# Optimization experiments

Hardware: AMD Instinct MI355X
Metric: run time of the kernel (lower is better)

## Reference

```python
import jax, jax.numpy as jnp
import numpy as np

N_NODES = 50000
NNZ = 1250000
N_EDGES = 1600000
VOCAB = 40000
HIDDEN = 128
LABELS = 2000
NUM_GCN = 2


def setup_inputs() -> dict:
    key = jax.random.key(0)
    ks = jax.random.split(key, 16)
    feat_ids = jax.random.randint(ks[0], (NNZ,), 0, VOCAB, dtype=jnp.int32)
    mid = jnp.sort(jax.random.randint(ks[1], (N_NODES - 1,), 0, NNZ, dtype=jnp.int32))
    offsets = jnp.concatenate([jnp.zeros((1,), jnp.int32), mid, jnp.full((1,), NNZ, jnp.int32)])
    feat_weights = jax.random.uniform(ks[2], (NNZ,), jnp.float32)
    edge_src = jax.random.randint(ks[3], (N_EDGES,), 0, N_NODES, dtype=jnp.int32)
    edge_dst = jax.random.randint(ks[4], (N_EDGES,), 0, N_NODES, dtype=jnp.int32)
    ppi_w = jax.random.uniform(ks[5], (N_EDGES,), jnp.float32)
    self_w = jax.random.uniform(ks[6], (N_EDGES,), jnp.float32)
    # learned params (xavier-ish scaling)
    emb_weight = jax.random.normal(ks[7], (VOCAB, HIDDEN), jnp.float32) * 0.02
    input_bias = jnp.zeros((HIDDEN,), jnp.float32)
    W1 = jax.random.normal(ks[8], (HIDDEN, HIDDEN), jnp.float32) * (1.0 / np.sqrt(HIDDEN))
    b1 = jnp.zeros((HIDDEN,), jnp.float32)
    W2 = jax.random.normal(ks[9], (HIDDEN, HIDDEN), jnp.float32) * (1.0 / np.sqrt(HIDDEN))
    b2 = jnp.zeros((HIDDEN,), jnp.float32)
    Wo = jax.random.normal(ks[10], (HIDDEN, LABELS), jnp.float32) * (1.0 / np.sqrt(HIDDEN))
    bo = jnp.zeros((LABELS,), jnp.float32)
    return {
        'feat_ids': feat_ids, 'offsets': offsets, 'feat_weights': feat_weights,
        'edge_src': edge_src, 'edge_dst': edge_dst, 'ppi_w': ppi_w, 'self_w': self_w,
        'emb_weight': emb_weight, 'input_bias': input_bias,
        'W1': W1, 'b1': b1, 'W2': W2, 'b2': b2, 'Wo': Wo, 'bo': bo,
    }


def _embedding_bag_sum(emb_weight, feat_ids, offsets, feat_weights):
    # EmbeddingBag(mode='sum', include_last_offset=True) with per_sample_weights:
    # bag b sums feat_weights[i] * emb_weight[feat_ids[i]] for i in [offsets[b], offsets[b+1]).
    bag_id = jnp.searchsorted(offsets, jnp.arange(NNZ, dtype=offsets.dtype), side='right') - 1
    vals = emb_weight[feat_ids] * feat_weights[:, None]  # [NNZ, H]
    return jax.ops.segment_sum(vals, bag_id, num_segments=N_NODES)  # [N, H]


def reference(feat_ids, offsets, feat_weights, edge_src, edge_dst, ppi_w, self_w,
              emb_weight, input_bias, W1, b1, W2, b2, Wo, bo):
    # input layer: EmbeddingBag sum + bias -> relu (dropout = identity in eval)
    h = jax.nn.relu(_embedding_bag_sum(emb_weight, feat_ids, offsets, feat_weights) + input_bias)
    for (W, b) in ((W1, b1), (W2, b2)):
        hs = h[edge_src]                                            # gather [E, H]
        res = jax.ops.segment_sum(hs * self_w[:, None], edge_dst, num_segments=N_NODES)
        agg = jax.ops.segment_sum(hs * ppi_w[:, None], edge_dst, num_segments=N_NODES)
        # NodeUpdate: dropout(relu(Linear(ppi_out))) + res  (dropout identity)
        h = jax.nn.relu(agg @ W + b) + res
    return h @ Wo + bo  # [N, LABELS]
```

## Files before the change

### kernel.cpp

```cpp
#include <hip/hip_runtime.h>

#define HID 128

typedef __bf16 bf16x8 __attribute__((ext_vector_type(8)));
typedef float f32x4 __attribute__((ext_vector_type(4)));

__device__ __forceinline__ unsigned short f2bf(float x) {
  unsigned int u = __builtin_bit_cast(unsigned int, x);
  u += 0x7FFFu + ((u >> 16) & 1u);
  return (unsigned short)(u >> 16);
}

__global__ void zero_int_kernel(int* __restrict__ p, int n) {
  int i = blockIdx.x * blockDim.x + threadIdx.x;
  if (i < n) p[i] = 0;
}

__global__ void degree_kernel(const int* __restrict__ dst, int* __restrict__ deg, int n) {
  int i = blockIdx.x * blockDim.x + threadIdx.x;
  if (i < n) atomicAdd(&deg[dst[i]], 1);
}

__global__ void __launch_bounds__(1024) scan_kernel(const int* __restrict__ deg,
                                                    int* __restrict__ eoff, int n) {
  __shared__ int ssum[1024];
  int t = threadIdx.x;
  int chunk = (n + 1023) / 1024;
  int beg = t * chunk;
  int end = min(beg + chunk, n);
  int s = 0;
  for (int i = beg; i < end; ++i) s += deg[i];
  ssum[t] = s;
  __syncthreads();
  for (int off = 1; off < 1024; off <<= 1) {
    int v = (t >= off) ? ssum[t - off] : 0;
    __syncthreads();
    ssum[t] += v;
    __syncthreads();
  }
  int base = (t == 0) ? 0 : ssum[t - 1];
  for (int i = beg; i < end; ++i) { eoff[i] = base; base += deg[i]; }
  if (t == 1023) eoff[n] = base;
}

__global__ void copy_int_kernel(const int* __restrict__ src, int* __restrict__ dst, int n) {
  int i = blockIdx.x * blockDim.x + threadIdx.x;
  if (i < n) dst[i] = src[i];
}

__global__ void scatter_kernel(const int* __restrict__ edst, const int* __restrict__ esrc,
                               const float* __restrict__ ppi, const float* __restrict__ selfw,
                               int* __restrict__ cursor,
                               int* __restrict__ esrc_s, float2* __restrict__ w2, int n) {
  int i = blockIdx.x * blockDim.x + threadIdx.x;
  if (i < n) {
    int d = edst[i];
    int pos = atomicAdd(&cursor[d], 1);
    esrc_s[pos] = esrc[i];
    w2[pos] = make_float2(ppi[i], selfw[i]);
  }
}

__global__ void __launch_bounds__(128) embed_kernel(const int* __restrict__ ids,
                                                    const int* __restrict__ offs,
                                                    const float* __restrict__ fw,
                                                    const float* __restrict__ emb,
                                                    const float* __restrict__ bias,
                                                    float* __restrict__ h) {
  int node = blockIdx.x;
  int t = threadIdx.x;
  int beg = offs[node], end = offs[node + 1];
  float acc = 0.f;
  int i = beg;
  for (; i + 8 <= end; i += 8) {
    int id[8];
    float w[8];
    float v[8];
#pragma unroll
    for (int u = 0; u < 8; ++u) id[u] = ids[i + u];
#pragma unroll
    for (int u = 0; u < 8; ++u) w[u] = fw[i + u];
#pragma unroll
    for (int u = 0; u < 8; ++u) v[u] = emb[(long)id[u] * HID + t];
#pragma unroll
    for (int u = 0; u < 8; ++u) acc += w[u] * v[u];
  }
  for (; i < end; ++i) {
    acc += fw[i] * emb[(long)ids[i] * HID + t];
  }
  acc += bias[t];
  h[(long)node * HID + t] = acc > 0.f ? acc : 0.f;
}

__global__ void __launch_bounds__(128) aggregate_kernel(const float* __restrict__ h,
                                                        const int* __restrict__ eoff,
                                                        const int* __restrict__ esrc_s,
                                                        const float2* __restrict__ w2,
                                                        float* __restrict__ agg,
                                                        float* __restrict__ res) {
  int node = blockIdx.x;
  int t = threadIdx.x;
  int beg = eoff[node], end = eoff[node + 1];
  float a = 0.f, r = 0.f;
  int j = beg;
  for (; j + 8 <= end; j += 8) {
    int s[8];
    float2 w[8];
    float v[8];
#pragma unroll
    for (int u = 0; u < 8; ++u) s[u] = esrc_s[j + u];
#pragma unroll
    for (int u = 0; u < 8; ++u) w[u] = w2[j + u];
#pragma unroll
    for (int u = 0; u < 8; ++u) v[u] = h[(long)s[u] * HID + t];
#pragma unroll
    for (int u = 0; u < 8; ++u) { a += w[u].x * v[u]; r += w[u].y * v[u]; }
  }
  for (; j < end; ++j) {
    int s = esrc_s[j];
    float2 w = w2[j];
    float v = h[(long)s * HID + t];
    a += w.x * v;
    r += w.y * v;
  }
  agg[(long)node * HID + t] = a;
  res[(long)node * HID + t] = r;
}

__global__ void __launch_bounds__(256) update_kernel(const float* __restrict__ agg,
                                                     const float* __restrict__ res,
                                                     const float* __restrict__ W,
                                                     const float* __restrict__ b,
                                                     float* __restrict__ hout, int n_nodes) {
  __shared__ __align__(16) float sW[HID * HID];
  __shared__ float sx[2][HID];
  int t = threadIdx.x & (HID - 1);
  int sub = threadIdx.x >> 7;
  for (int i = threadIdx.x; i < HID * HID / 4; i += 256)
    ((float4*)sW)[i] = ((const float4*)W)[i];
  float bias = b[t];
  __syncthreads();
  for (int node0 = blockIdx.x * 2; node0 < n_nodes; node0 += gridDim.x * 2) {
    int node = node0 + sub;
    bool valid = node < n_nodes;
    if (valid) sx[sub][t] = agg[(long)node * HID + t];
    __syncthreads();
    if (valid) {
      float acc = 0.f;
#pragma unroll 16
      for (int k = 0; k < HID; ++k) acc += sx[sub][k] * sW[k * HID + t];
      float v = acc + bias;
      v = v > 0.f ? v : 0.f;
      hout[(long)node * HID + t] = v + res[(long)node * HID + t];
    }
    __syncthreads();
  }
}

__global__ void transpose_wo_kernel(const float* __restrict__ Wo,
                                    unsigned short* __restrict__ WoT, int labels) {
  int idx = blockIdx.x * 256 + threadIdx.x;
  if (idx < labels * HID) {
    int n = idx >> 7, k = idx & (HID - 1);
    WoT[idx] = f2bf(Wo[(long)k * labels + n]);
  }
}

#define LDK 136

__global__ void __launch_bounds__(256) out_gemm_kernel(const float* __restrict__ h,
                                                       const unsigned short* __restrict__ WoT,
                                                       const float* __restrict__ bo,
                                                       float* __restrict__ out,
                                                       int n_nodes, int labels) {
  __shared__ __align__(16) unsigned short sA[64 * LDK];
  __shared__ __align__(16) unsigned short sB[80 * LDK];
  int m0 = blockIdx.x * 64;
  int n0 = blockIdx.y * 80;
  int tid = threadIdx.x;

  for (int i = tid; i < 64 * 32; i += 256) {
    int r = i >> 5, c4 = i & 31;
    int row = m0 + r;
    if (row >= n_nodes) row = n_nodes - 1;
    float4 v = ((const float4*)(h + (long)row * HID))[c4];
    ushort4 bb;
    bb.x = f2bf(v.x); bb.y = f2bf(v.y); bb.z = f2bf(v.z); bb.w = f2bf(v.w);
    *(ushort4*)&sA[r * LDK + c4 * 4] = bb;
  }
  for (int i = tid; i < 80 * 32; i += 256) {
    int r = i >> 5, c4 = i & 31;
    ushort4 v = ((const ushort4*)(WoT + (long)(n0 + r) * HID))[c4];
    *(ushort4*)&sB[r * LDK + c4 * 4] = v;
  }
  __syncthreads();

  int wave = tid >> 6, lane = tid & 63;
  int lrow = lane & 15, quad = lane >> 4;
  f32x4 acc[5];
#pragma unroll
  for (int c = 0; c < 5; ++c) acc[c] = (f32x4){0.f, 0.f, 0.f, 0.f};

#pragma unroll
  for (int kk = 0; kk < 4; ++kk) {
    bf16x8 af = *(const bf16x8*)&sA[(wave * 16 + lrow) * LDK + kk * 32 + quad * 8];
#pragma unroll
    for (int c = 0; c < 5; ++c) {
      bf16x8 bf = *(const bf16x8*)&sB[(c * 16 + lrow) * LDK + kk * 32 + quad * 8];
      acc[c] = __builtin_amdgcn_mfma_f32_16x16x32_bf16(af, bf, acc[c], 0, 0, 0);
    }
  }

#pragma unroll
  for (int c = 0; c < 5; ++c) {
    int n = n0 + c * 16 + lrow;
    float bias = bo[n];
#pragma unroll
    for (int r = 0; r < 4; ++r) {
      int m = m0 + wave * 16 + quad * 4 + r;
      if (m < n_nodes) out[(long)m * labels + n] = acc[c][r] + bias;
    }
  }
}

extern "C" void kernel_launch(void* const* d_in, const int* in_sizes, int n_in,
                              void* d_out, int out_size, void* d_ws, size_t ws_size,
                              hipStream_t stream) {
  const int* feat_ids = (const int*)d_in[0];
  const int* offsets = (const int*)d_in[1];
  const float* feat_w = (const float*)d_in[2];
  const int* esrc = (const int*)d_in[3];
  const int* edst = (const int*)d_in[4];
  const float* ppi = (const float*)d_in[5];
  const float* selfw = (const float*)d_in[6];
  const float* emb = (const float*)d_in[7];
  const float* ibias = (const float*)d_in[8];
  const float* W1 = (const float*)d_in[9];
  const float* b1 = (const float*)d_in[10];
  const float* W2 = (const float*)d_in[11];
  const float* b2 = (const float*)d_in[12];
  const float* Wo = (const float*)d_in[13];
  const float* bo = (const float*)d_in[14];
  float* out = (float*)d_out;

  int N = in_sizes[1] - 1;
  int E = in_sizes[3];
  int LABELS = in_sizes[14];

  char* ws = (char*)d_ws;
  size_t HN = (size_t)N * HID;
  float* h0 = (float*)ws;                    ws += HN * 4;
  float* agg = (float*)ws;                   ws += HN * 4;
  float* res = (float*)ws;                   ws += HN * 4;
  unsigned short* WoT = (unsigned short*)ws; ws += (size_t)LABELS * HID * 2;
  float2* w2 = (float2*)ws;                  ws += (size_t)E * 8;
  int* deg = (int*)ws;                       ws += (size_t)N * 4;
  int* eoff = (int*)ws;                      ws += (size_t)(N + 1) * 4;
  int* cursor = (int*)ws;                    ws += (size_t)N * 4;
  int* esrc_s = (int*)ws;                    ws += (size_t)E * 4;

  zero_int_kernel<<<(N + 255) / 256, 256, 0, stream>>>(deg, N);
  degree_kernel<<<(E + 255) / 256, 256, 0, stream>>>(edst, deg, E);
  scan_kernel<<<1, 1024, 0, stream>>>(deg, eoff, N);
  copy_int_kernel<<<(N + 255) / 256, 256, 0, stream>>>(eoff, cursor, N);
  scatter_kernel<<<(E + 255) / 256, 256, 0, stream>>>(edst, esrc, ppi, selfw,
                                                      cursor, esrc_s, w2, E);

  embed_kernel<<<N, HID, 0, stream>>>(feat_ids, offsets, feat_w, emb, ibias, h0);
  transpose_wo_kernel<<<(LABELS * HID + 255) / 256, 256, 0, stream>>>(Wo, WoT, LABELS);

  aggregate_kernel<<<N, HID, 0, stream>>>(h0, eoff, esrc_s, w2, agg, res);
  update_kernel<<<1024, 256, 0, stream>>>(agg, res, W1, b1, h0, N);
  aggregate_kernel<<<N, HID, 0, stream>>>(h0, eoff, esrc_s, w2, agg, res);
  update_kernel<<<1024, 256, 0, stream>>>(agg, res, W2, b2, h0, N);

  dim3 g((N + 63) / 64, LABELS / 80);
  out_gemm_kernel<<<g, 256, 0, stream>>>(h0, WoT, bo, out, N, LABELS);
}
```

Baseline: 1.421 ms.

## Store node features and embedding table in bf16; pack edge records into int4

Converts the embedding table and the node hidden states to bf16, so the embedding-bag and aggregation gathers move half the bytes. Each wavefront now handles one node with two features per lane. Edge source, ppi weight and self weight are packed into a single 16-byte record so one load fetches all three. The output GEMM reads the bf16 hidden state directly instead of converting from fp32. The cost is an extra cast pass over the embedding table and reduced precision in the intermediate activations, including the residual term.

New measurement: 1.281 ms. 9.8% less time.

```diff
diff --git a/kernel.cpp b/kernel.cpp
--- a/kernel.cpp
+++ b/kernel.cpp
@@ -9,6 +9,9 @@
   unsigned int u = __builtin_bit_cast(unsigned int, x);
   u += 0x7FFFu + ((u >> 16) & 1u);
   return (unsigned short)(u >> 16);
+}
+__device__ __forceinline__ float bf2f(unsigned short x) {
+  return __builtin_bit_cast(float, (unsigned int)x << 16);
 }
 
 __global__ void zero_int_kernel(int* __restrict__ p, int n) {
@@ -50,88 +53,111 @@
 
 __global__ void scatter_kernel(const int* __restrict__ edst, const int* __restrict__ esrc,
                                const float* __restrict__ ppi, const float* __restrict__ selfw,
-                               int* __restrict__ cursor,
-                               int* __restrict__ esrc_s, float2* __restrict__ w2, int n) {
+                               int* __restrict__ cursor, int4* __restrict__ edges, int n) {
   int i = blockIdx.x * blockDim.x + threadIdx.x;
   if (i < n) {
     int d = edst[i];
     int pos = atomicAdd(&cursor[d], 1);
-    esrc_s[pos] = esrc[i];
-    w2[pos] = make_float2(ppi[i], selfw[i]);
-  }
-}
-
-__global__ void __launch_bounds__(128) embed_kernel(const int* __restrict__ ids,
+    edges[pos] = make_int4(esrc[i], __builtin_bit_cast(int, ppi[i]),
+                           __builtin_bit_cast(int, selfw[i]), 0);
+  }
+}
+
+__global__ void cast_emb_kernel(const float* __restrict__ emb,
+                                unsigned short* __restrict__ embb, int n) {
+  int i = blockIdx.x * blockDim.x + threadIdx.x;
+  if (i < n) embb[i] = f2bf(emb[i]);
+}
+
+__global__ void __launch_bounds__(256) embed_kernel(const int* __restrict__ ids,
                                                     const int* __restrict__ offs,
                                                     const float* __restrict__ fw,
-                                                    const float* __restrict__ emb,
+                                                    const unsigned int* __restrict__ embb,
                                                     const float* __restrict__ bias,
-                                                    float* __restrict__ h) {
-  int node = blockIdx.x;
-  int t = threadIdx.x;
+                                                    unsigned int* __restrict__ hb, int n_nodes) {
+  int node = blockIdx.x * 4 + (threadIdx.x >> 6);
+  if (node >= n_nodes) return;
+  int u = threadIdx.x & 63;
   int beg = offs[node], end = offs[node + 1];
-  float acc = 0.f;
+  float a0 = 0.f, a1 = 0.f;
   int i = beg;
   for (; i + 8 <= end; i += 8) {
     int id[8];
     float w[8];
-    float v[8];
-#pragma unroll
-    for (int u = 0; u < 8; ++u) id[u] = ids[i + u];
-#pragma unroll
-    for (int u = 0; u < 8; ++u) w[u] = fw[i + u];
-#pragma unroll
-    for (int u = 0; u < 8; ++u) v[u] = emb[(long)id[u] * HID + t];
-#pragma unroll
-    for (int u = 0; u < 8; ++u) acc += w[u] * v[u];
+    unsigned int v[8];
+#pragma unroll
+    for (int q = 0; q < 8; ++q) id[q] = ids[i + q];
+#pragma unroll
+    for (int q = 0; q < 8; ++q) w[q] = fw[i + q];
+#pragma unroll
+    for (int q = 0; q < 8; ++q) v[q] = embb[(long)id[q] * 64 + u];
+#pragma unroll
+    for (int q = 0; q < 8; ++q) {
+      a0 += w[q] * bf2f((unsigned short)(v[q] & 0xffffu));
+      a1 += w[q] * bf2f((unsigned short)(v[q] >> 16));
+    }
   }
   for (; i < end; ++i) {
-    acc += fw[i] * emb[(long)ids[i] * HID + t];
-  }
-  acc += bias[t];
-  h[(long)node * HID + t] = acc > 0.f ? acc : 0.f;
-}
-
-__global__ void __launch_bounds__(128) aggregate_kernel(const float* __restrict__ h,
+    unsigned int v = embb[(long)ids[i] * 64 + u];
+    float w = fw[i];
+    a0 += w * bf2f((unsigned short)(v & 0xffffu));
+    a1 += w * bf2f((unsigned short)(v >> 16));
+  }
+  a0 += bias[2 * u];
+  a1 += bias[2 * u + 1];
+  a0 = a0 > 0.f ? a0 : 0.f;
+  a1 = a1 > 0.f ? a1 : 0.f;
+  hb[(long)node * 64 + u] = (unsigned int)f2bf(a0) | ((unsigned int)f2bf(a1) << 16);
+}
+
+__global__ void __launch_bounds__(256) aggregate_kernel(const unsigned int* __restrict__ hb,
                                                         const int* __restrict__ eoff,
-                                                        const int* __restrict__ esrc_s,
-                                                        const float2* __restrict__ w2,
-                                                        float* __restrict__ agg,
-                                                        float* __restrict__ res) {
-  int node = blockIdx.x;
-  int t = threadIdx.x;
+                                                        const int4* __restrict__ edges,
+                                                        float2* __restrict__ agg,
+                                                        float2* __restrict__ res, int n_nodes) {
+  int node = blockIdx.x * 4 + (threadIdx.x >> 6);
+  if (node >= n_nodes) return;
+  int u = threadIdx.x & 63;
   int beg = eoff[node], end = eoff[node + 1];
-  float a = 0.f, r = 0.f;
+  float a0 = 0.f, a1 = 0.f, r0 = 0.f, r1 = 0.f;
   int j = beg;
   for (; j + 8 <= end; j += 8) {
-    int s[8];
-    float2 w[8];
-    float v[8];
-#pragma unroll
-    for (int u = 0; u < 8; ++u) s[u] = esrc_s[j + u];
-#pragma unroll
-    for (int u = 0; u < 8; ++u) w[u] = w2[j + u];
-#pragma unroll
-    for (int u = 0; u < 8; ++u) v[u] = h[(long)s[u] * HID + t];
-#pragma unroll
-    for (int u = 0; u < 8; ++u) { a += w[u].x * v[u]; r += w[u].y * v[u]; }
+    int4 e[8];
+    unsigned int v[8];
+#pragma unroll
+    for (int q = 0; q < 8; ++q) e[q] = edges[j + q];
+#pragma unroll
+    for (int q = 0; q < 8; ++q) v[q] = hb[(long)e[q].x * 64 + u];
+#pragma unroll
+    for (int q = 0; q < 8; ++q) {
+      float lo = bf2f((unsigned short)(v[q] & 0xffffu));
+      float hi = bf2f((unsigned short)(v[q] >> 16));
+      float wp = __builtin_bit_cast(float, e[q].y);
+      float ws = __builtin_bit_cast(float, e[q].z);
+      a0 += wp * lo; a1 += wp * hi;
+      r0 += ws * lo; r1 += ws * hi;
+    }
   }
   for (; j < end; ++j) {
-    int s = esrc_s[j];
-    float2 w = w2[j];
-    float v = h[(long)s * HID + t];
-    a += w.x * v;
-    r += w.y * v;
-  }
-  agg[(long)node * HID + t] = a;
-  res[(long)node * HID + t] = r;
+    int4 e = edges[j];
+    unsigned int v = hb[(long)e.x * 64 + u];
+    float lo = bf2f((unsigned short)(v & 0xffffu));
+    float hi = bf2f((unsigned short)(v >> 16));
+    float wp = __builtin_bit_cast(float, e.y);
+    float ws = __builtin_bit_cast(float, e.z);
+    a0 += wp * lo; a1 += wp * hi;
+    r0 += ws * lo; r1 += ws * hi;
+  }
+  agg[(long)node * 64 + u] = make_float2(a0, a1);
+  res[(long)node * 64 + u] = make_float2(r0, r1);
 }
 
 __global__ void __launch_bounds__(256) update_kernel(const float* __restrict__ agg,
                                                      const float* __restrict__ res,
                                                      const float* __restrict__ W,
                                                      const float* __restrict__ b,
-                                                     float* __restrict__ hout, int n_nodes) {
+                                                     unsigned short* __restrict__ hout,
+                                                     int n_nodes) {
   __shared__ __align__(16) float sW[HID * HID];
   __shared__ float sx[2][HID];
   int t = threadIdx.x & (HID - 1);
@@ -151,7 +177,7 @@
       for (int k = 0; k < HID; ++k) acc += sx[sub][k] * sW[k * HID + t];
       float v = acc + bias;
       v = v > 0.f ? v : 0.f;
-      hout[(long)node * HID + t] = v + res[(long)node * HID + t];
+      hout[(long)node * HID + t] = f2bf(v + res[(long)node * HID + t]);
     }
     __syncthreads();
   }
@@ -168,7 +194,7 @@
 
 #define LDK 136
 
-__global__ void __launch_bounds__(256) out_gemm_kernel(const float* __restrict__ h,
+__global__ void __launch_bounds__(256) out_gemm_kernel(const unsigned short* __restrict__ hb,
                                                        const unsigned short* __restrict__ WoT,
                                                        const float* __restrict__ bo,
                                                        float* __restrict__ out,
@@ -183,10 +209,8 @@
     int r = i >> 5, c4 = i & 31;
     int row = m0 + r;
     if (row >= n_nodes) row = n_nodes - 1;
-    float4 v = ((const float4*)(h + (long)row * HID))[c4];
-    ushort4 bb;
-    bb.x = f2bf(v.x); bb.y = f2bf(v.y); bb.z = f2bf(v.z); bb.w = f2bf(v.w);
-    *(ushort4*)&sA[r * LDK + c4 * 4] = bb;
+    ushort4 v = ((const ushort4*)(hb + (long)row * HID))[c4];
+    *(ushort4*)&sA[r * LDK + c4 * 4] = v;
   }
   for (int i = tid; i < 80 * 32; i += 256) {
     int r = i >> 5, c4 = i & 31;
@@ -245,35 +269,41 @@
 
   int N = in_sizes[1] - 1;
   int E = in_sizes[3];
+  int EMBN = in_sizes[7];
   int LABELS = in_sizes[14];
 
   char* ws = (char*)d_ws;
   size_t HN = (size_t)N * HID;
-  float* h0 = (float*)ws;                    ws += HN * 4;
-  float* agg = (float*)ws;                   ws += HN * 4;
-  float* res = (float*)ws;                   ws += HN * 4;
-  unsigned short* WoT = (unsigned short*)ws; ws += (size_t)LABELS * HID * 2;
-  float2* w2 = (float2*)ws;                  ws += (size_t)E * 8;
-  int* deg = (int*)ws;                       ws += (size_t)N * 4;
-  int* eoff = (int*)ws;                      ws += (size_t)(N + 1) * 4;
-  int* cursor = (int*)ws;                    ws += (size_t)N * 4;
-  int* esrc_s = (int*)ws;                    ws += (size_t)E * 4;
+  unsigned short* h_bf = (unsigned short*)ws;  ws += HN * 2;
+  float* agg = (float*)ws;                     ws += HN * 4;
+  float* res = (float*)ws;                     ws += HN * 4;
+  unsigned short* WoT = (unsigned short*)ws;   ws += (size_t)LABELS * HID * 2;
+  unsigned short* embb = (unsigned short*)ws;  ws += (size_t)EMBN * 2;
+  int4* edges = (int4*)ws;                     ws += (size_t)E * 16;
+  int* deg = (int*)ws;                         ws += (size_t)N * 4;
+  int* eoff = (int*)ws;                        ws += (size_t)(N + 1) * 4;
+  int* cursor = (int*)ws;                      ws += (size_t)N * 4;
 
   zero_int_kernel<<<(N + 255) / 256, 256, 0, stream>>>(deg, N);
   degree_kernel<<<(E + 255) / 256, 256, 0, stream>>>(edst, deg, E);
   scan_kernel<<<1, 1024, 0, stream>>>(deg, eoff, N);
   copy_int_kernel<<<(N + 255) / 256, 256, 0, stream>>>(eoff, cursor, N);
   scatter_kernel<<<(E + 255) / 256, 256, 0, stream>>>(edst, esrc, ppi, selfw,
-                                                      cursor, esrc_s, w2, E);
-
-  embed_kernel<<<N, HID, 0, stream>>>(feat_ids, offsets, feat_w, emb, ibias, h0);
+                                                      cursor, edges, E);
+
+  cast_emb_kernel<<<(EMBN + 255) / 256, 256, 0, stream>>>(emb, embb, EMBN);
+  embed_kernel<<<(N + 3) / 4, 256, 0, stream>>>(feat_ids, offsets, feat_w,
+                                                (const unsigned int*)embb, ibias,
+                                                (unsigned int*)h_bf, N);
   transpose_wo_kernel<<<(LABELS * HID + 255) / 256, 256, 0, stream>>>(Wo, WoT, LABELS);
 
-  aggregate_kernel<<<N, HID, 0, stream>>>(h0, eoff, esrc_s, w2, agg, res);
-  update_kernel<<<1024, 256, 0, stream>>>(agg, res, W1, b1, h0, N);
-  aggregate_kernel<<<N, HID, 0, stream>>>(h0, eoff, esrc_s, w2, agg, res);
-  update_kernel<<<1024, 256, 0, stream>>>(agg, res, W2, b2, h0, N);
+  aggregate_kernel<<<(N + 3) / 4, 256, 0, stream>>>((const unsigned int*)h_bf, eoff, edges,
+                                                    (float2*)agg, (float2*)res, N);
+  update_kernel<<<1024, 256, 0, stream>>>(agg, res, W1, b1, h_bf, N);
+  aggregate_kernel<<<(N + 3) / 4, 256, 0, stream>>>((const unsigned int*)h_bf, eoff, edges,
+                                                    (float2*)agg, (float2*)res, N);
+  update_kernel<<<1024, 256, 0, stream>>>(agg, res, W2, b2, h_bf, N);
 
   dim3 g((N + 63) / 64, LABELS / 80);
-  out_gemm_kernel<<<g, 256, 0, stream>>>(h0, WoT, bo, out, N, LABELS);
-}
+  out_gemm_kernel<<<g, 256, 0, stream>>>(h_bf, WoT, bo, out, N, LABELS);
+}
```
